# Kernel tuning notes

Measured on AMD Instinct MI355X. Metric: run time of the kernel, lower is better.

The kernel has to match this reference:

```python
import jax, jax.numpy as jnp
import numpy as np

B, S, D = 4, 2048, 1024

def setup_inputs() -> dict:
    key = jax.random.key(0)
    ks = jax.random.split(key, 7)
    s = 1.0 / np.sqrt(D)
    return {
        "x":  jax.random.normal(ks[0], (B, S, D), dtype=jnp.float32),
        "Wq": jax.random.uniform(ks[1], (D, D), jnp.float32, -s, s),
        "bq": jax.random.uniform(ks[2], (D,),  jnp.float32, -s, s),
        "Wk": jax.random.uniform(ks[3], (D, D), jnp.float32, -s, s),
        "bk": jax.random.uniform(ks[4], (D,),  jnp.float32, -s, s),
        "Wv": jax.random.uniform(ks[5], (D, D), jnp.float32, -s, s),
        "bv": jax.random.uniform(ks[6], (D,),  jnp.float32, -s, s),
    }

def reference(x, Wq, bq, Wk, bk, Wv, bv):
    # Q/K/V projections: [B,S,D]
    Q = jnp.einsum('bsd,de->bse', x, Wq) + bq
    K = jnp.einsum('bsd,de->bse', x, Wk) + bk
    V = jnp.einsum('bsd,de->bse', x, Wv) + bv
    scale = 1.0 / jnp.sqrt(jnp.asarray(K.shape[-1], K.dtype))
    scores = jnp.einsum('bqd,bkd->bqk', Q, K) * scale  # [B,S,S]
    weights = jax.nn.softmax(scores, axis=-1)
    return jnp.einsum('bqk,bkd->bqd', weights, V)
```

## Files before the change

kernel.cpp:

```cpp
#include <hip/hip_runtime.h>

typedef __attribute__((ext_vector_type(4))) float f32x4;
typedef __attribute__((ext_vector_type(8))) short bf16x8;

__device__ __forceinline__ float bf2f(unsigned short u) {
  union { unsigned int i; float f; } x; x.i = ((unsigned int)u) << 16; return x.f;
}
__device__ __forceinline__ unsigned short f2bf(float f) {
  union { float f; unsigned int i; } x; x.f = f;
  unsigned int r = (x.i + 0x7FFFu + ((x.i >> 16) & 1u)) >> 16;
  return (unsigned short)r;
}

#define BARX __builtin_amdgcn_s_barrier()
#define VM0  asm volatile("s_waitcnt vmcnt(0)" ::: "memory")
#define GLD(gsrc, ldsoff)                                                        \
  __builtin_amdgcn_global_load_lds(                                              \
      (const __attribute__((address_space(1))) void*)(gsrc),                     \
      (__attribute__((address_space(3))) void*)&lds[ldsoff], 16, 0, 0)

__global__ __launch_bounds__(256) void cvt_f2b(const float* __restrict__ src,
                                               unsigned short* __restrict__ dst, long n4) {
  long i = (long)blockIdx.x * 256 + threadIdx.x;
  long stride = (long)gridDim.x * 256;
  for (; i < n4; i += stride) {
    float4 v = *(const float4*)&src[i * 4];
    ushort4 o;
    o.x = f2bf(v.x); o.y = f2bf(v.y); o.z = f2bf(v.z); o.w = f2bf(v.w);
    *(ushort4*)&dst[i * 4] = o;
  }
}

__global__ __launch_bounds__(256) void transpose_f2b(const float* __restrict__ src,
                                                     unsigned short* __restrict__ dst,
                                                     int rows, int cols) {
  __shared__ float t[32][33];
  int bx = blockIdx.x * 32, by = blockIdx.y * 32;
  int tx = threadIdx.x, ty = threadIdx.y;
#pragma unroll
  for (int k = 0; k < 4; ++k)
    t[ty + 8 * k][tx] = src[(long)(by + ty + 8 * k) * cols + bx + tx];
  __syncthreads();
#pragma unroll
  for (int k = 0; k < 4; ++k)
    dst[(long)(bx + ty + 8 * k) * rows + by + tx] = f2bf(t[tx][ty + 8 * k]);
}

template <int MODE>
__global__ __launch_bounds__(256, 2) void gemmo(const unsigned short* __restrict__ Ap_,
                                                const unsigned short* __restrict__ Bp_,
                                                void* __restrict__ Cv,
                                                void* __restrict__ vtv,
                                                const float* __restrict__ q_,
                                                const float* __restrict__ k_,
                                                const float* __restrict__ v_,
                                                int Kd, int lda, int ldb, int ldc, float scale,
                                                long sA, long sB, long sC) {
  __shared__ unsigned short lds[16384];
  int bx, by, bz;
  if (MODE == 2) {
    const int flat = blockIdx.x;
    const int nid = ((flat & 7) << 6) | (flat >> 3);
    bx = nid & 15; by = (nid >> 4) & 7; bz = nid >> 7;
  } else {
    bx = blockIdx.x; by = blockIdx.y; bz = blockIdx.z;
  }
  const int tid = threadIdx.x;
  const int m0 = bx * 128, n0 = by * 128;
  const int lane = tid & 63, wave = tid >> 6;
  const int wm = wave >> 1, wn = wave & 1;
  const int rr = tid >> 3;
  const int cSrc = ((tid & 7) ^ (rr & 7)) << 3;
  const int lc = lane & 15, lr = lane >> 4;
  const int x0 = (lc & 4) << 3;
  const int x1 = 32 ^ x0;
  const int klo = (lr << 3) ^ ((lc & 3) << 3);
  const int aoff = (wm * 64 + lc) * 64 + klo;
  const int boff = 8192 + (wn * 64 + lc) * 64 + klo;
  const int NT = Kd >> 6;

  const unsigned short* pA = Ap_ + (long)bz * sA + (long)(m0 + rr) * lda + cSrc;
  const unsigned short* pB = Bp_ + (long)bz * sB + (long)(n0 + rr) * ldb + cSrc;
  const long a32 = (long)32 * lda, b32 = (long)32 * ldb;

  f32x4 acc[4][4] = {};
  f32x4 es[4] = {};
  bf16x8 ones;
#pragma unroll
  for (int j = 0; j < 8; ++j) ones[j] = (short)0x3F80;

  for (int t = 0; t < NT; ++t) {
    GLD(pA, tid * 8);                  GLD(pA + a32, 2048 + tid * 8);
    GLD(pA + 2 * a32, 4096 + tid * 8); GLD(pA + 3 * a32, 6144 + tid * 8);
    GLD(pB, 8192 + tid * 8);           GLD(pB + b32, 10240 + tid * 8);
    GLD(pB + 2 * b32, 12288 + tid * 8); GLD(pB + 3 * b32, 14336 + tid * 8);
    VM0;
    BARX;
    bf16x8 a0[2][2], a1[2][2], bb[4][2];
#pragma unroll
    for (int ni = 0; ni < 4; ++ni) {
      bb[ni][0] = *(const bf16x8*)&lds[boff + ni * 1024 + x0];
      bb[ni][1] = *(const bf16x8*)&lds[boff + ni * 1024 + x1];
    }
#pragma unroll
    for (int mi = 0; mi < 2; ++mi) {
      a0[mi][0] = *(const bf16x8*)&lds[aoff + mi * 1024 + x0];
      a0[mi][1] = *(const bf16x8*)&lds[aoff + mi * 1024 + x1];
    }
    __builtin_amdgcn_s_setprio(1);
#pragma unroll
    for (int mi = 0; mi < 2; ++mi)
#pragma unroll
      for (int ni = 0; ni < 4; ++ni)
#pragma unroll
        for (int x = 0; x < 2; ++x)
          acc[mi][ni] = __builtin_amdgcn_mfma_f32_16x16x32_bf16(
              a0[mi][x], bb[ni][x], acc[mi][ni], 0, 0, 0);
    if (MODE == 2) {
#pragma unroll
      for (int mi = 0; mi < 2; ++mi)
#pragma unroll
        for (int x = 0; x < 2; ++x)
          es[mi] = __builtin_amdgcn_mfma_f32_16x16x32_bf16(a0[mi][x], ones, es[mi], 0, 0, 0);
    }
    __builtin_amdgcn_s_setprio(0);
#pragma unroll
    for (int mi = 0; mi < 2; ++mi) {
      a1[mi][0] = *(const bf16x8*)&lds[aoff + 2048 + mi * 1024 + x0];
      a1[mi][1] = *(const bf16x8*)&lds[aoff + 2048 + mi * 1024 + x1];
    }
    __builtin_amdgcn_s_setprio(1);
#pragma unroll
    for (int mi = 0; mi < 2; ++mi)
#pragma unroll
      for (int ni = 0; ni < 4; ++ni)
#pragma unroll
        for (int x = 0; x < 2; ++x)
          acc[2 + mi][ni] = __builtin_amdgcn_mfma_f32_16x16x32_bf16(
              a1[mi][x], bb[ni][x], acc[2 + mi][ni], 0, 0, 0);
    if (MODE == 2) {
#pragma unroll
      for (int mi = 0; mi < 2; ++mi)
#pragma unroll
        for (int x = 0; x < 2; ++x)
          es[2 + mi] = __builtin_amdgcn_mfma_f32_16x16x32_bf16(a1[mi][x], ones, es[2 + mi], 0, 0, 0);
    }
    __builtin_amdgcn_s_setprio(0);
    BARX;
    pA += 64; pB += 64;
  }

  const int r0 = m0 + wm * 64 + lr * 4;
  const int c0 = n0 + wn * 64 + lc;
  if (MODE == 2) {
    float* O = (float*)Cv + (long)bz * sC;
#pragma unroll
    for (int mi = 0; mi < 4; ++mi)
#pragma unroll
      for (int r = 0; r < 4; ++r) {
        const float iv = 1.0f / es[mi][r];
#pragma unroll
        for (int ni = 0; ni < 4; ++ni)
          O[(long)(r0 + mi * 16 + r) * ldc + (c0 + ni * 16)] = acc[mi][ni][r] * iv;
      }
  } else if (MODE == 0 && n0 >= 2048) {
    unsigned short* VTp = (unsigned short*)vtv + (long)(m0 >> 11) * 1024 * 2064;
    const int sl = (m0 & 2047) + wm * 64 + lr * 4;
#pragma unroll
    for (int ni = 0; ni < 4; ++ni) {
      const int d = c0 - 2048 + ni * 16;
      const float bv = v_[d];
#pragma unroll
      for (int mi = 0; mi < 4; ++mi)
#pragma unroll
        for (int r = 0; r < 4; ++r)
          VTp[(long)d * 2064 + (sl + mi * 16 + r)] = f2bf(acc[mi][ni][r] + bv);
    }
  } else {
    unsigned short* C = (unsigned short*)Cv + (long)bz * sC;
#pragma unroll
    for (int ni = 0; ni < 4; ++ni) {
      const int col = c0 + ni * 16;
      float bv = 0.0f;
      if (MODE == 0) bv = (col < 1024) ? q_[col] : k_[col - 1024];
#pragma unroll
      for (int mi = 0; mi < 4; ++mi)
#pragma unroll
        for (int r = 0; r < 4; ++r) {
          float val = acc[mi][ni][r];
          val = (MODE == 0) ? (val + bv) : __expf(val * scale);
          C[(long)(r0 + mi * 16 + r) * ldc + col] = f2bf(val);
        }
    }
  }
}

extern "C" void kernel_launch(void* const* d_in, const int* in_sizes, int n_in,
                              void* d_out, int out_size, void* d_ws, size_t ws_size,
                              hipStream_t stream) {
  const float* x  = (const float*)d_in[0];
  const float* Wq = (const float*)d_in[1];
  const float* bq = (const float*)d_in[2];
  const float* Wk = (const float*)d_in[3];
  const float* bk = (const float*)d_in[4];
  const float* Wv = (const float*)d_in[5];
  const float* bv = (const float*)d_in[6];
  float* out = (float*)d_out;

  const int Bb = 4, S = 2048, D = 1024;
  const long MS = (long)Bb * S;
  const int LDQ = 2080;
  const int LDP = 2064;

  char* ws = (char*)d_ws;
  unsigned short* xb = (unsigned short*)(ws);
  unsigned short* Wt = (unsigned short*)(ws + (16L << 20));
  unsigned short* QK = (unsigned short*)(ws + (33L << 20));
  unsigned short* VT = (unsigned short*)(ws + (66L << 20));
  unsigned short* Sc = (unsigned short*)(ws);

  cvt_f2b<<<2048, 256, 0, stream>>>(x, xb, MS * D / 4);

  dim3 tb(32, 8);
  dim3 tg(D / 32, D / 32);
  transpose_f2b<<<tg, tb, 0, stream>>>(Wq, Wt, D, D);
  transpose_f2b<<<tg, tb, 0, stream>>>(Wk, Wt + 1024 * 1024, D, D);
  transpose_f2b<<<tg, tb, 0, stream>>>(Wv, Wt + 2 * 1024 * 1024, D, D);

  dim3 pgrid(MS / 128, 3072 / 128, 1);
  gemmo<0><<<pgrid, 256, 0, stream>>>(xb, Wt, QK, VT, bq, bk, bv,
                                      D, D, D, LDQ, 1.0f, 0, 0, 0);

  dim3 sgrid(S / 128, S / 128, Bb);
  gemmo<1><<<sgrid, 256, 0, stream>>>(QK, QK + 1024, Sc, nullptr, nullptr, nullptr, nullptr,
                                      D, LDQ, LDQ, LDP, 1.0f / 32.0f,
                                      (long)S * LDQ, (long)S * LDQ, (long)S * LDP);

  gemmo<2><<<512, 256, 0, stream>>>(Sc, VT, out, nullptr, nullptr, nullptr, nullptr,
                                    2048, LDP, LDP, D, 1.0f,
                                    (long)S * LDP, (long)D * LDP, (long)S * D);
}
```

Measured before the change: 171.9 us.

## Shrink GEMM blocks to 64x128 tiles with two waves and merge weight transposes

Each GEMM block changes from a 128x128 tile with four waves to a 64x128 tile with two waves, and every wave now covers all 64 rows. Grid sizes double, LDS use drops to 24KB, and the load pattern changes to 16-row strides. This aims to put more blocks on each CU and balance the work better across the GPU, at the cost of less reuse of A/B data and more global traffic per output. The three weight-transpose launches are also merged into one launch with a z dimension.

```diff
diff --git a/kernel.cpp b/kernel.cpp
--- a/kernel.cpp
+++ b/kernel.cpp
@@ -31,23 +31,26 @@
   }
 }
 
-__global__ __launch_bounds__(256) void transpose_f2b(const float* __restrict__ src,
-                                                     unsigned short* __restrict__ dst,
-                                                     int rows, int cols) {
+__global__ __launch_bounds__(256) void transpose_w(const float* __restrict__ Wq,
+                                                   const float* __restrict__ Wk,
+                                                   const float* __restrict__ Wv,
+                                                   unsigned short* __restrict__ dst) {
   __shared__ float t[32][33];
+  const float* src = (blockIdx.z == 0) ? Wq : (blockIdx.z == 1) ? Wk : Wv;
+  unsigned short* d = dst + (long)blockIdx.z * 1024 * 1024;
   int bx = blockIdx.x * 32, by = blockIdx.y * 32;
   int tx = threadIdx.x, ty = threadIdx.y;
 #pragma unroll
   for (int k = 0; k < 4; ++k)
-    t[ty + 8 * k][tx] = src[(long)(by + ty + 8 * k) * cols + bx + tx];
+    t[ty + 8 * k][tx] = src[(long)(by + ty + 8 * k) * 1024 + bx + tx];
   __syncthreads();
 #pragma unroll
   for (int k = 0; k < 4; ++k)
-    dst[(long)(bx + ty + 8 * k) * rows + by + tx] = f2bf(t[tx][ty + 8 * k]);
+    d[(long)(bx + ty + 8 * k) * 1024 + by + tx] = f2bf(t[tx][ty + 8 * k]);
 }
 
 template <int MODE>
-__global__ __launch_bounds__(256, 2) void gemmo(const unsigned short* __restrict__ Ap_,
+__global__ __launch_bounds__(128, 2) void gemmo(const unsigned short* __restrict__ Ap_,
                                                 const unsigned short* __restrict__ Bp_,
                                                 void* __restrict__ Cv,
                                                 void* __restrict__ vtv,
@@ -56,32 +59,31 @@
                                                 const float* __restrict__ v_,
                                                 int Kd, int lda, int ldb, int ldc, float scale,
                                                 long sA, long sB, long sC) {
-  __shared__ unsigned short lds[16384];
+  __shared__ unsigned short lds[12288];
   int bx, by, bz;
   if (MODE == 2) {
     const int flat = blockIdx.x;
-    const int nid = ((flat & 7) << 6) | (flat >> 3);
-    bx = nid & 15; by = (nid >> 4) & 7; bz = nid >> 7;
+    const int nid = ((flat & 7) << 7) | (flat >> 3);
+    bx = nid & 31; by = (nid >> 5) & 7; bz = nid >> 8;
   } else {
     bx = blockIdx.x; by = blockIdx.y; bz = blockIdx.z;
   }
   const int tid = threadIdx.x;
-  const int m0 = bx * 128, n0 = by * 128;
+  const int m0 = bx * 64, n0 = by * 128;
   const int lane = tid & 63, wave = tid >> 6;
-  const int wm = wave >> 1, wn = wave & 1;
   const int rr = tid >> 3;
   const int cSrc = ((tid & 7) ^ (rr & 7)) << 3;
   const int lc = lane & 15, lr = lane >> 4;
   const int x0 = (lc & 4) << 3;
   const int x1 = 32 ^ x0;
   const int klo = (lr << 3) ^ ((lc & 3) << 3);
-  const int aoff = (wm * 64 + lc) * 64 + klo;
-  const int boff = 8192 + (wn * 64 + lc) * 64 + klo;
+  const int aoff = lc * 64 + klo;
+  const int boff = 4096 + (wave * 64 + lc) * 64 + klo;
   const int NT = Kd >> 6;
 
   const unsigned short* pA = Ap_ + (long)bz * sA + (long)(m0 + rr) * lda + cSrc;
   const unsigned short* pB = Bp_ + (long)bz * sB + (long)(n0 + rr) * ldb + cSrc;
-  const long a32 = (long)32 * lda, b32 = (long)32 * ldb;
+  const long a16 = (long)16 * lda, b16 = (long)16 * ldb;
 
   f32x4 acc[4][4] = {};
   f32x4 es[4] = {};
@@ -90,10 +92,10 @@
   for (int j = 0; j < 8; ++j) ones[j] = (short)0x3F80;
 
   for (int t = 0; t < NT; ++t) {
-    GLD(pA, tid * 8);                  GLD(pA + a32, 2048 + tid * 8);
-    GLD(pA + 2 * a32, 4096 + tid * 8); GLD(pA + 3 * a32, 6144 + tid * 8);
-    GLD(pB, 8192 + tid * 8);           GLD(pB + b32, 10240 + tid * 8);
-    GLD(pB + 2 * b32, 12288 + tid * 8); GLD(pB + 3 * b32, 14336 + tid * 8);
+#pragma unroll
+    for (int j = 0; j < 4; ++j) GLD(pA + j * a16, j * 1024 + tid * 8);
+#pragma unroll
+    for (int j = 0; j < 8; ++j) GLD(pB + j * b16, 4096 + j * 1024 + tid * 8);
     VM0;
     BARX;
     bf16x8 a0[2][2], a1[2][2], bb[4][2];
@@ -150,8 +152,8 @@
     pA += 64; pB += 64;
   }
 
-  const int r0 = m0 + wm * 64 + lr * 4;
-  const int c0 = n0 + wn * 64 + lc;
+  const int r0 = m0 + lr * 4;
+  const int c0 = n0 + wave * 64 + lc;
   if (MODE == 2) {
     float* O = (float*)Cv + (long)bz * sC;
 #pragma unroll
@@ -165,7 +167,7 @@
       }
   } else if (MODE == 0 && n0 >= 2048) {
     unsigned short* VTp = (unsigned short*)vtv + (long)(m0 >> 11) * 1024 * 2064;
-    const int sl = (m0 & 2047) + wm * 64 + lr * 4;
+    const int sl = (m0 & 2047) + lr * 4;
 #pragma unroll
     for (int ni = 0; ni < 4; ++ni) {
       const int d = c0 - 2048 + ni * 16;
@@ -222,21 +224,19 @@
   cvt_f2b<<<2048, 256, 0, stream>>>(x, xb, MS * D / 4);
 
   dim3 tb(32, 8);
-  dim3 tg(D / 32, D / 32);
-  transpose_f2b<<<tg, tb, 0, stream>>>(Wq, Wt, D, D);
-  transpose_f2b<<<tg, tb, 0, stream>>>(Wk, Wt + 1024 * 1024, D, D);
-  transpose_f2b<<<tg, tb, 0, stream>>>(Wv, Wt + 2 * 1024 * 1024, D, D);
-
-  dim3 pgrid(MS / 128, 3072 / 128, 1);
-  gemmo<0><<<pgrid, 256, 0, stream>>>(xb, Wt, QK, VT, bq, bk, bv,
+  dim3 tg(D / 32, D / 32, 3);
+  transpose_w<<<tg, tb, 0, stream>>>(Wq, Wk, Wv, Wt);
+
+  dim3 pgrid(MS / 64, 3072 / 128, 1);
+  gemmo<0><<<pgrid, 128, 0, stream>>>(xb, Wt, QK, VT, bq, bk, bv,
                                       D, D, D, LDQ, 1.0f, 0, 0, 0);
 
-  dim3 sgrid(S / 128, S / 128, Bb);
-  gemmo<1><<<sgrid, 256, 0, stream>>>(QK, QK + 1024, Sc, nullptr, nullptr, nullptr, nullptr,
+  dim3 sgrid(S / 64, S / 128, Bb);
+  gemmo<1><<<sgrid, 128, 0, stream>>>(QK, QK + 1024, Sc, nullptr, nullptr, nullptr, nullptr,
                                       D, LDQ, LDQ, LDP, 1.0f / 32.0f,
                                       (long)S * LDQ, (long)S * LDQ, (long)S * LDP);
 
-  gemmo<2><<<512, 256, 0, stream>>>(Sc, VT, out, nullptr, nullptr, nullptr, nullptr,
-                                    2048, LDP, LDP, D, 1.0f,
-                                    (long)S * LDP, (long)D * LDP, (long)S * D);
-}
+  gemmo<2><<<1024, 128, 0, stream>>>(Sc, VT, out, nullptr, nullptr, nullptr, nullptr,
+                                     2048, LDP, LDP, D, 1.0f,
+                                     (long)S * LDP, (long)D * LDP, (long)S * D);
+}
```

Result: slower. 207.9 us (+21.0%).
